# Kernel tuning notes

Hardware: AMD Instinct MI355X
Metric: run time of the kernel (lower is better)

The kernel has to match this reference:

```python
import jax, jax.numpy as jnp
import numpy as np

HIDDEN = 64
NUM_LAYERS = 6
BN_EPS = 1e-5


def setup_inputs() -> dict:
    key = jax.random.key(0)
    N, M = 1024, 1024
    num_nodes = N + M
    ks = jax.random.split(key, 12)
    x = jax.random.normal(ks[0], (num_nodes, 2), dtype=jnp.float32)
    # complete bipartite edges: (a, N+b) for all a in [0,N), b in [0,M), row-major so view(N,M) is meaningful
    row = jnp.repeat(jnp.arange(N, dtype=jnp.int64), M)
    col = N + jnp.tile(jnp.arange(M, dtype=jnp.int64), N)
    edge_index = jnp.stack([row, col], axis=0)
    s = 1.0 / np.sqrt(HIDDEN)
    return {
        "x": x,
        "edge_index": edge_index,
        "in_w": jax.random.normal(ks[1], (2, HIDDEN), jnp.float32) * 0.5,
        "in_b": jnp.zeros((HIDDEN,), jnp.float32),
        "conv_w": jax.random.normal(ks[2], (NUM_LAYERS, HIDDEN, HIDDEN), jnp.float32) * s,
        "conv_b": jnp.zeros((NUM_LAYERS, HIDDEN), jnp.float32),
        "bn_gamma": jnp.ones((NUM_LAYERS, HIDDEN), jnp.float32),
        "bn_beta": jnp.zeros((NUM_LAYERS, HIDDEN), jnp.float32),
        "out_w": jax.random.normal(ks[3], (2 * HIDDEN, 1), jnp.float32) * s,
        "out_b": jnp.zeros((1,), jnp.float32),
        "N": N,
        "M": M,
    }


def reference(x, edge_index, in_w, in_b, conv_w, conv_b, bn_gamma, bn_beta, out_w, out_b, N, M):
    num_nodes = x.shape[0]
    # GCN normalization with added self-loops (PyG GCNConv defaults)
    loops = jnp.arange(num_nodes, dtype=edge_index.dtype)
    row = jnp.concatenate([edge_index[0], loops])
    col = jnp.concatenate([edge_index[1], loops])
    deg = jax.ops.segment_sum(jnp.ones_like(col, dtype=x.dtype), col, num_segments=num_nodes)
    dinv = jnp.where(deg > 0, jax.lax.rsqrt(deg), 0.0)
    norm = dinv[row] * dinv[col]  # [E+num_nodes]

    h = jax.nn.relu(x @ in_w + in_b)
    for i in range(NUM_LAYERS):
        h_res = h
        hw = h @ conv_w[i]
        agg = jax.ops.segment_sum(hw[row] * norm[:, None], col, num_segments=num_nodes)
        h = agg + conv_b[i]
        # BatchNorm1d in training mode: batch stats, biased variance
        mu = h.mean(axis=0)
        var = ((h - mu) ** 2).mean(axis=0)
        h = (h - mu) * jax.lax.rsqrt(var + BN_EPS) * bn_gamma[i] + bn_beta[i]
        h = jax.nn.relu(h)
        if i > 0 and i % 2 == 1:
            h = h + h_res

    ef = jnp.concatenate([h[edge_index[0]], h[edge_index[1]]], axis=1)  # [E, 2H]
    scores = (ef @ out_w + out_b)[:, 0]
    return scores.reshape(N, M)
```

## Files before the change

### kernel.cpp

```cpp
#include <hip/hip_runtime.h>


#define NBLK 32
#define MAGIC 0x13572468u

__device__ __forceinline__ float relu_(float x) { return x > 0.f ? x : 0.f; }

#define AT_LOAD(p)    __hip_atomic_load((p), __ATOMIC_RELAXED, __HIP_MEMORY_SCOPE_AGENT)
#define AT_STORE(p,v) __hip_atomic_store((p), (v), __ATOMIC_RELAXED, __HIP_MEMORY_SCOPE_AGENT)
#define AT_ADD(p,v)   __hip_atomic_fetch_add((p), (v), __ATOMIC_RELAXED, __HIP_MEMORY_SCOPE_AGENT)

#define PART_OFF  256
#define UV_OFF    6400
#define FLAG_OFF  8448

__global__ __launch_bounds__(256, 1) void k_fused(
    const float* __restrict__ x,
    const float* __restrict__ in_w, const float* __restrict__ in_b,
    const float* __restrict__ conv_w,
    const float* __restrict__ bn_g, const float* __restrict__ bn_b,
    const float* __restrict__ out_w,
    unsigned int* __restrict__ ws)
{
    __shared__ float Wl[2][4096];
    __shared__ float hl[64 * 68];
    __shared__ float sredS[4 * 64], sredQ[4 * 64];
    __shared__ float stat[256];
    __shared__ float pcoef[64], scoef[64];
    __shared__ float g_lds[384], b_lds[384];
    __shared__ float ow_lds[128];

    const int t = threadIdx.x, b = blockIdx.x;
    const int p  = t >> 3;
    const int fi = t & 7;
    const int f0 = fi * 8;
    const int r0 = p, r1 = p + 32;
    const int node0 = b * 64 + p, node1 = node0 + 32;
    const bool isA = b < 16;
    float* part = (float*)(ws + PART_OFF);
    float* uv   = (float*)(ws + UV_OFF);

    {
        const float4* src = (const float4*)conv_w;
        float4* dst = (float4*)Wl[0];
        dst[t]       = src[t];
        dst[t + 256] = src[t + 256];
        dst[t + 512] = src[t + 512];
        dst[t + 768] = src[t + 768];
        for (int i = t; i < 384; i += 256) { g_lds[i] = bn_g[i]; b_lds[i] = bn_b[i]; }
        if (t < 128) ow_lds[t] = out_w[t];
    }

    if (b == 0) {
        for (int i = t; i < 6400; i += 256) AT_STORE(ws + i, 0u);
        asm volatile("s_waitcnt vmcnt(0)" ::: "memory");
        __syncthreads();
        if (t == 0) AT_STORE(ws + FLAG_OFF, MAGIC);
    }

    {
        float x0 = x[node0 * 2], x1 = x[node0 * 2 + 1];
        float y0 = x[node1 * 2], y1 = x[node1 * 2 + 1];
#pragma unroll
        for (int j = 0; j < 8; j++) {
            int f = f0 + j;
            float wa = in_w[f], wb = in_w[64 + f], bb = in_b[f];
            hl[r0 * 68 + f] = relu_(fmaf(x0, wa, fmaf(x1, wb, bb)));
            hl[r1 * 68 + f] = relu_(fmaf(y0, wa, fmaf(y1, wb, bb)));
        }
    }
    __syncthreads();

    for (int layer = 0; layer < 6; layer++) {
        float4 pf0, pf1, pf2, pf3;
        if (layer < 5) {
            const float4* src = (const float4*)(conv_w + (layer + 1) * 4096);
            pf0 = src[t];
            pf1 = src[t + 256];
            pf2 = src[t + 512];
            pf3 = src[t + 768];
        }

        const float* Wb = Wl[layer & 1];
        float acc0[8], acc1[8];
#pragma unroll
        for (int j = 0; j < 8; j++) { acc0[j] = 0.f; acc1[j] = 0.f; }

#pragma unroll 4
        for (int k = 0; k < 64; k += 4) {
            float4 ha = *(const float4*)&hl[r0 * 68 + k];
            float4 hb = *(const float4*)&hl[r1 * 68 + k];
            float hav[4] = {ha.x, ha.y, ha.z, ha.w};
            float hbv[4] = {hb.x, hb.y, hb.z, hb.w};
#pragma unroll
            for (int j = 0; j < 4; j++) {
                const float* wr = Wb + (k + j) * 64 + f0;
                float4 w0 = *(const float4*)wr;
                float4 w1 = *(const float4*)(wr + 4);
                float wv[8] = {w0.x, w0.y, w0.z, w0.w, w1.x, w1.y, w1.z, w1.w};
#pragma unroll
                for (int q = 0; q < 8; q++) {
                    acc0[q] = fmaf(hav[j], wv[q], acc0[q]);
                    acc1[q] = fmaf(hbv[j], wv[q], acc1[q]);
                }
            }
        }

        if (layer < 5) {
            float4* dst = (float4*)Wl[(layer + 1) & 1];
            dst[t]       = pf0;
            dst[t + 256] = pf1;
            dst[t + 512] = pf2;
            dst[t + 768] = pf3;
        }

        {
            float sv[8], qv[8];
#pragma unroll
            for (int j = 0; j < 8; j++) {
                sv[j] = acc0[j] + acc1[j];
                qv[j] = fmaf(acc0[j], acc0[j], acc1[j] * acc1[j]);
            }
#pragma unroll
            for (int m = 8; m < 64; m <<= 1) {
#pragma unroll
                for (int j = 0; j < 8; j++) {
                    sv[j] += __shfl_xor(sv[j], m);
                    qv[j] += __shfl_xor(qv[j], m);
                }
            }
            int w = t >> 6, lane = t & 63;
            if (lane < 8) {
#pragma unroll
                for (int j = 0; j < 8; j++) {
                    sredS[w * 64 + lane * 8 + j] = sv[j];
                    sredQ[w * 64 + lane * 8 + j] = qv[j];
                }
            }
        }
        if (layer == 0) {
            __syncthreads();
            if (t == 0) while (AT_LOAD(ws + FLAG_OFF) != MAGIC) {}
        }
        __syncthreads();

        if (t < 64) {
            float S = sredS[t] + sredS[64 + t] + sredS[128 + t] + sredS[192 + t];
            float Q = sredQ[t] + sredQ[64 + t] + sredQ[128 + t] + sredQ[192 + t];
            float* base = part + layer * 1024 + (b & 3) * 256 + (isA ? 0 : 128);
            AT_ADD(base + t, S);
            AT_ADD(base + 64 + t, Q);
            asm volatile("s_waitcnt vmcnt(0)" ::: "memory");
            if (t == 0) {
                AT_ADD(ws + layer * 32, 1u);
                const unsigned int* c = ws + layer * 32;
                for (;;) {
                    unsigned a0 = AT_LOAD(c);
                    unsigned a1 = AT_LOAD(c);
                    unsigned a2 = AT_LOAD(c);
                    unsigned a3 = AT_LOAD(c);
                    if (a0 >= NBLK) break;
                    if (a1 >= NBLK) break;
                    if (a2 >= NBLK) break;
                    if (a3 >= NBLK) break;
                }
            }
        }
        __syncthreads();

        {
            const float* pp = part + layer * 1024 + t;
            float s = AT_LOAD(pp) + AT_LOAD(pp + 256) + AT_LOAD(pp + 512) + AT_LOAD(pp + 768);
            stat[t] = s;
        }
        __syncthreads();

        if (t < 64) {
            float SA = stat[t], QA = stat[64 + t], SB = stat[128 + t], QB = stat[192 + t];
            const float c1 = 9.75609756097561e-4f;
            const float c2 = 3.1234752377721214e-2f;
            float sumAgg = SA + c1 * SB + 1024.f * c2 * SA;
            float sumSq  = QA + c1 * c1 * QB + 2.f * c1 * c2 * SA * SB
                         + 1024.f * c2 * c2 * SA * SA;
            float meanAgg = sumAgg * (1.f / 2048.f);
            float var = sumSq * (1.f / 2048.f) - meanAgg * meanAgg;
            float rstd = rsqrtf(var + 1e-5f);
            float scale = rstd * g_lds[layer * 64 + t];
            float bt = b_lds[layer * 64 + t];
            if (isA) { pcoef[t] = scale;      scoef[t] = bt - meanAgg * scale; }
            else     { pcoef[t] = c1 * scale; scoef[t] = bt + (c2 * SA - meanAgg) * scale; }
        }
        __syncthreads();

        float v0[8], v1[8];
#pragma unroll
        for (int j = 0; j < 8; j++) {
            float pc = pcoef[f0 + j], sc = scoef[f0 + j];
            v0[j] = relu_(fmaf(acc0[j], pc, sc));
            v1[j] = relu_(fmaf(acc1[j], pc, sc));
        }
        if (layer == 1 || layer == 3 || layer == 5) {
#pragma unroll
            for (int j = 0; j < 8; j++) {
                v0[j] += hl[r0 * 68 + f0 + j];
                v1[j] += hl[r1 * 68 + f0 + j];
            }
        }

        if (layer < 5) {
            __syncthreads();
#pragma unroll
            for (int j = 0; j < 8; j++) {
                hl[r0 * 68 + f0 + j] = v0[j];
                hl[r1 * 68 + f0 + j] = v1[j];
            }
            __syncthreads();
        } else {
            const float* w = ow_lds + (isA ? 0 : 64) + f0;
            float d0 = 0.f, d1 = 0.f;
#pragma unroll
            for (int j = 0; j < 8; j++) {
                d0 = fmaf(v0[j], w[j], d0);
                d1 = fmaf(v1[j], w[j], d1);
            }
            d0 += __shfl_xor(d0, 1); d1 += __shfl_xor(d1, 1);
            d0 += __shfl_xor(d0, 2); d1 += __shfl_xor(d1, 2);
            d0 += __shfl_xor(d0, 4); d1 += __shfl_xor(d1, 4);
            if (fi == 0) {
                AT_STORE(uv + node0, d0);
                AT_STORE(uv + node1, d1);
            }
        }
    }
}

__global__ __launch_bounds__(256) void k_out(const float* __restrict__ uv,
                                             const float* __restrict__ out_b,
                                             float* __restrict__ out) {
    const int a = blockIdx.x;
    const int t = threadIdx.x;
    float ua = uv[a] + out_b[0];
    float4 vv = ((const float4*)(uv + 1024))[t];
    ((float4*)(out + a * 1024))[t] =
        make_float4(ua + vv.x, ua + vv.y, ua + vv.z, ua + vv.w);
}

extern "C" void kernel_launch(void* const* d_in, const int* in_sizes, int n_in,
                              void* d_out, int out_size, void* d_ws, size_t ws_size,
                              hipStream_t stream) {
    const float* x      = (const float*)d_in[0];
    const float* in_w   = (const float*)d_in[2];
    const float* in_b   = (const float*)d_in[3];
    const float* conv_w = (const float*)d_in[4];
    const float* bn_g   = (const float*)d_in[6];
    const float* bn_b   = (const float*)d_in[7];
    const float* out_w  = (const float*)d_in[8];
    const float* out_b  = (const float*)d_in[9];
    float* out = (float*)d_out;

    unsigned int* ws = (unsigned int*)d_ws;
    const float* uv = (const float*)(ws + UV_OFF);

    k_fused<<<NBLK, 256, 0, stream>>>(x, in_w, in_b, conv_w, bn_g, bn_b,
                                      out_w, ws);
    k_out<<<1024, 256, 0, stream>>>(uv, out_b, out);
}
```

Measured before the change: 115.7 us.

## Split fused GCN across 64 half-size blocks and compute BN coefficients per wave

Doubles the block count to 64 and halves each block to 128 threads and 32 nodes, so more CUs share the per-layer work. Each wave now reads the global partial sums and derives the BN scale and shift itself, passing them between lanes with shuffles instead of staging stat, pcoef and scoef in LDS. This drops two __syncthreads per layer. The workspace layout is compacted: the ready flag moves to ws[0], the counters to CNT_OFF, and fewer words are zeroed. The grid barrier now waits on 64 arrivals, and each block loads more of the weight matrix per thread.

```diff
diff --git a/kernel.cpp b/kernel.cpp
--- a/kernel.cpp
+++ b/kernel.cpp
@@ -1,7 +1,7 @@
 #include <hip/hip_runtime.h>
 
 
-#define NBLK 32
+#define NBLK 64
 #define MAGIC 0x13572468u
 
 __device__ __forceinline__ float relu_(float x) { return x > 0.f ? x : 0.f; }
@@ -10,11 +10,11 @@
 #define AT_STORE(p,v) __hip_atomic_store((p), (v), __ATOMIC_RELAXED, __HIP_MEMORY_SCOPE_AGENT)
 #define AT_ADD(p,v)   __hip_atomic_fetch_add((p), (v), __ATOMIC_RELAXED, __HIP_MEMORY_SCOPE_AGENT)
 
+#define CNT_OFF   64
 #define PART_OFF  256
 #define UV_OFF    6400
-#define FLAG_OFF  8448
-
-__global__ __launch_bounds__(256, 1) void k_fused(
+
+__global__ __launch_bounds__(128, 1) void k_fused(
     const float* __restrict__ x,
     const float* __restrict__ in_w, const float* __restrict__ in_b,
     const float* __restrict__ conv_w,
@@ -23,10 +23,8 @@
     unsigned int* __restrict__ ws)
 {
     __shared__ float Wl[2][4096];
-    __shared__ float hl[64 * 68];
-    __shared__ float sredS[4 * 64], sredQ[4 * 64];
-    __shared__ float stat[256];
-    __shared__ float pcoef[64], scoef[64];
+    __shared__ float hl[32 * 68];
+    __shared__ float sredS[2 * 64], sredQ[2 * 64];
     __shared__ float g_lds[384], b_lds[384];
     __shared__ float ow_lds[128];
 
@@ -34,28 +32,29 @@
     const int p  = t >> 3;
     const int fi = t & 7;
     const int f0 = fi * 8;
-    const int r0 = p, r1 = p + 32;
-    const int node0 = b * 64 + p, node1 = node0 + 32;
-    const bool isA = b < 16;
+    const int lane = t & 63;
+    const int wv = t >> 6;
+    const int r0 = p, r1 = p + 16;
+    const int node0 = b * 32 + p, node1 = node0 + 16;
+    const bool isA = b < 32;
     float* part = (float*)(ws + PART_OFF);
     float* uv   = (float*)(ws + UV_OFF);
 
     {
         const float4* src = (const float4*)conv_w;
         float4* dst = (float4*)Wl[0];
-        dst[t]       = src[t];
-        dst[t + 256] = src[t + 256];
-        dst[t + 512] = src[t + 512];
-        dst[t + 768] = src[t + 768];
-        for (int i = t; i < 384; i += 256) { g_lds[i] = bn_g[i]; b_lds[i] = bn_b[i]; }
+#pragma unroll
+        for (int i = 0; i < 8; i++) dst[t + i * 128] = src[t + i * 128];
+        for (int i = t; i < 384; i += 128) { g_lds[i] = bn_g[i]; b_lds[i] = bn_b[i]; }
         if (t < 128) ow_lds[t] = out_w[t];
     }
 
     if (b == 0) {
-        for (int i = t; i < 6400; i += 256) AT_STORE(ws + i, 0u);
+        for (int i = t; i < 192; i += 128) AT_STORE(ws + CNT_OFF + i, 0u);
+        for (int i = t; i < 6144; i += 128) AT_STORE(ws + PART_OFF + i, 0u);
         asm volatile("s_waitcnt vmcnt(0)" ::: "memory");
         __syncthreads();
-        if (t == 0) AT_STORE(ws + FLAG_OFF, MAGIC);
+        if (t == 0) AT_STORE(ws, MAGIC);
     }
 
     {
@@ -72,13 +71,11 @@
     __syncthreads();
 
     for (int layer = 0; layer < 6; layer++) {
-        float4 pf0, pf1, pf2, pf3;
+        float4 pf[8];
         if (layer < 5) {
             const float4* src = (const float4*)(conv_w + (layer + 1) * 4096);
-            pf0 = src[t];
-            pf1 = src[t + 256];
-            pf2 = src[t + 512];
-            pf3 = src[t + 768];
+#pragma unroll
+            for (int i = 0; i < 8; i++) pf[i] = src[t + i * 128];
         }
 
         const float* Wb = Wl[layer & 1];
@@ -97,21 +94,19 @@
                 const float* wr = Wb + (k + j) * 64 + f0;
                 float4 w0 = *(const float4*)wr;
                 float4 w1 = *(const float4*)(wr + 4);
-                float wv[8] = {w0.x, w0.y, w0.z, w0.w, w1.x, w1.y, w1.z, w1.w};
+                float wv8[8] = {w0.x, w0.y, w0.z, w0.w, w1.x, w1.y, w1.z, w1.w};
 #pragma unroll
                 for (int q = 0; q < 8; q++) {
-                    acc0[q] = fmaf(hav[j], wv[q], acc0[q]);
-                    acc1[q] = fmaf(hbv[j], wv[q], acc1[q]);
+                    acc0[q] = fmaf(hav[j], wv8[q], acc0[q]);
+                    acc1[q] = fmaf(hbv[j], wv8[q], acc1[q]);
                 }
             }
         }
 
         if (layer < 5) {
             float4* dst = (float4*)Wl[(layer + 1) & 1];
-            dst[t]       = pf0;
-            dst[t + 256] = pf1;
-            dst[t + 512] = pf2;
-            dst[t + 768] = pf3;
+#pragma unroll
+            for (int i = 0; i < 8; i++) dst[t + i * 128] = pf[i];
         }
 
         {
@@ -129,31 +124,31 @@
                     qv[j] += __shfl_xor(qv[j], m);
                 }
             }
-            int w = t >> 6, lane = t & 63;
             if (lane < 8) {
 #pragma unroll
                 for (int j = 0; j < 8; j++) {
-                    sredS[w * 64 + lane * 8 + j] = sv[j];
-                    sredQ[w * 64 + lane * 8 + j] = qv[j];
-                }
-            }
-        }
+                    sredS[wv * 64 + lane * 8 + j] = sv[j];
+                    sredQ[wv * 64 + lane * 8 + j] = qv[j];
+                }
+            }
+        }
+        __syncthreads();
+
         if (layer == 0) {
+            if (t == 0) while (AT_LOAD(ws) != MAGIC) {}
             __syncthreads();
-            if (t == 0) while (AT_LOAD(ws + FLAG_OFF) != MAGIC) {}
-        }
-        __syncthreads();
-
-        if (t < 64) {
-            float S = sredS[t] + sredS[64 + t] + sredS[128 + t] + sredS[192 + t];
-            float Q = sredQ[t] + sredQ[64 + t] + sredQ[128 + t] + sredQ[192 + t];
+        }
+
+        if (wv == 0) {
+            float S = sredS[lane] + sredS[64 + lane];
+            float Q = sredQ[lane] + sredQ[64 + lane];
             float* base = part + layer * 1024 + (b & 3) * 256 + (isA ? 0 : 128);
-            AT_ADD(base + t, S);
-            AT_ADD(base + 64 + t, Q);
+            AT_ADD(base + lane, S);
+            AT_ADD(base + 64 + lane, Q);
             asm volatile("s_waitcnt vmcnt(0)" ::: "memory");
-            if (t == 0) {
-                AT_ADD(ws + layer * 32, 1u);
-                const unsigned int* c = ws + layer * 32;
+            if (lane == 0) {
+                AT_ADD(ws + CNT_OFF + layer * 32, 1u);
+                const unsigned int* c = ws + CNT_OFF + layer * 32;
                 for (;;) {
                     unsigned a0 = AT_LOAD(c);
                     unsigned a1 = AT_LOAD(c);
@@ -168,15 +163,18 @@
         }
         __syncthreads();
 
+        float pc_f, sc_f;
         {
-            const float* pp = part + layer * 1024 + t;
-            float s = AT_LOAD(pp) + AT_LOAD(pp + 256) + AT_LOAD(pp + 512) + AT_LOAD(pp + 768);
-            stat[t] = s;
-        }
-        __syncthreads();
-
-        if (t < 64) {
-            float SA = stat[t], QA = stat[64 + t], SB = stat[128 + t], QB = stat[192 + t];
+            const float* base = part + layer * 1024;
+            float SA = 0.f, QA = 0.f, SB = 0.f, QB = 0.f;
+#pragma unroll
+            for (int r = 0; r < 4; r++) {
+                const float* rb = base + r * 256;
+                SA += AT_LOAD(rb + lane);
+                QA += AT_LOAD(rb + 64 + lane);
+                SB += AT_LOAD(rb + 128 + lane);
+                QB += AT_LOAD(rb + 192 + lane);
+            }
             const float c1 = 9.75609756097561e-4f;
             const float c2 = 3.1234752377721214e-2f;
             float sumAgg = SA + c1 * SB + 1024.f * c2 * SA;
@@ -185,17 +183,17 @@
             float meanAgg = sumAgg * (1.f / 2048.f);
             float var = sumSq * (1.f / 2048.f) - meanAgg * meanAgg;
             float rstd = rsqrtf(var + 1e-5f);
-            float scale = rstd * g_lds[layer * 64 + t];
-            float bt = b_lds[layer * 64 + t];
-            if (isA) { pcoef[t] = scale;      scoef[t] = bt - meanAgg * scale; }
-            else     { pcoef[t] = c1 * scale; scoef[t] = bt + (c2 * SA - meanAgg) * scale; }
-        }
-        __syncthreads();
+            float scale = rstd * g_lds[layer * 64 + lane];
+            float bt = b_lds[layer * 64 + lane];
+            if (isA) { pc_f = scale;      sc_f = bt - meanAgg * scale; }
+            else     { pc_f = c1 * scale; sc_f = bt + (c2 * SA - meanAgg) * scale; }
+        }
 
         float v0[8], v1[8];
 #pragma unroll
         for (int j = 0; j < 8; j++) {
-            float pc = pcoef[f0 + j], sc = scoef[f0 + j];
+            float pc = __shfl(pc_f, f0 + j);
+            float sc = __shfl(sc_f, f0 + j);
             v0[j] = relu_(fmaf(acc0[j], pc, sc));
             v1[j] = relu_(fmaf(acc1[j], pc, sc));
         }
@@ -208,7 +206,6 @@
         }
 
         if (layer < 5) {
-            __syncthreads();
 #pragma unroll
             for (int j = 0; j < 8; j++) {
                 hl[r0 * 68 + f0 + j] = v0[j];
@@ -261,7 +258,7 @@
     unsigned int* ws = (unsigned int*)d_ws;
     const float* uv = (const float*)(ws + UV_OFF);
 
-    k_fused<<<NBLK, 256, 0, stream>>>(x, in_w, in_b, conv_w, bn_g, bn_b,
+    k_fused<<<NBLK, 128, 0, stream>>>(x, in_w, in_b, conv_w, bn_g, bn_b,
                                       out_w, ws);
     k_out<<<1024, 256, 0, stream>>>(uv, out_b, out);
 }
```

After: 115.6 us. No clear change (-0.1%).
